# Performance work log

Measured on AMD Instinct MI355X. Metric: run time of the kernel, lower is better.

The kernel has to match this reference:

```python
import jax, jax.numpy as jnp
import numpy as np

NUM_HEADS = 8
EPS = 1e-5


def setup_inputs() -> dict:
    key = jax.random.key(0)
    ks = jax.random.split(key, 6)
    B, C, H, W = 8, 256, 32, 32
    s = 1.0 / np.sqrt(C)  # fan-in scale for 1x1 conv weights
    return {
        "x": jax.random.normal(ks[0], (B, C, H, W), jnp.float32),
        "Wq": jax.random.normal(ks[1], (C, C), jnp.float32) * s,
        "bq": jnp.zeros((C,), jnp.float32),
        "Wk": jax.random.normal(ks[2], (C, C), jnp.float32) * s,
        "bk": jnp.zeros((C,), jnp.float32),
        "Wv": jax.random.normal(ks[3], (C, C), jnp.float32) * s,
        "bv": jnp.zeros((C,), jnp.float32),
        "Wp": jax.random.normal(ks[4], (C, C), jnp.float32) * s,
        "bp": jnp.zeros((C,), jnp.float32),
        "gamma": jnp.ones((C,), jnp.float32),
        "beta": jnp.zeros((C,), jnp.float32),
    }


def _conv1x1(x, W, b):
    # 1x1 Conv2d == channel-mixing matmul: [B,C,H,W] -> [B,C,H,W]
    return jnp.einsum('oi,bihw->bohw', W, x) + b[None, :, None, None]


def reference(x, Wq, bq, Wk, bk, Wv, bv, Wp, bp, gamma, beta):
    B, C, H, W = x.shape
    nh = NUM_HEADS
    hd = C // nh
    HW = H * W

    q = _conv1x1(x, Wq, bq).reshape(B, nh, hd, HW)
    k = _conv1x1(x, Wk, bk).reshape(B, nh, hd, HW)
    v = _conv1x1(x, Wv, bv).reshape(B, nh, hd, HW)

    scores = jnp.einsum('bhdi,bhdj->bhij', q, k) / (hd ** 0.5)  # [B,nh,HW,HW]
    attn = jax.nn.softmax(scores, axis=-1)
    out = jnp.einsum('bhij,bhdj->bhdi', attn, v).reshape(B, C, H, W)

    out = _conv1x1(out, Wp, bp) + x  # residual

    # LayerNorm over channel dim (channels-last, as in original)
    o = out.transpose(0, 2, 3, 1)  # [B,H,W,C]
    mu = jnp.mean(o, axis=-1, keepdims=True)
    var = jnp.var(o, axis=-1, keepdims=True)
    o = (o - mu) * jax.lax.rsqrt(var + EPS) * gamma + beta
    return o.transpose(0, 3, 1, 2)
```

## Files before the change

kernel.cpp:

```cpp
#include <hip/hip_runtime.h>
#include <math.h>

#define NB 8
#define NC 256
#define NHW 1024
#define NHEADS 8
#define HD 32

typedef _Float16 half_t;
typedef __attribute__((ext_vector_type(8))) _Float16 half8;
typedef __attribute__((ext_vector_type(2))) _Float16 half2v;
typedef __attribute__((ext_vector_type(4))) float floatx4;

__device__ __forceinline__ half2v pk2(float a, float b) {
    union {
        __fp16 __attribute__((ext_vector_type(2))) r;
        half2v h;
    } u;
    u.r = __builtin_amdgcn_cvt_pkrtz(a, b);
    return u.h;
}
__device__ __forceinline__ void st8h(half_t* p, half2v a, half2v b) {
    union { half2v h[2]; uint2 u; } t;
    t.h[0] = a; t.h[1] = b;
    *(uint2*)p = t.u;
}

__global__ __launch_bounds__(256) void prepx(
    const float* __restrict__ Wq, const float* __restrict__ Wk,
    const float* __restrict__ Wv, const float* __restrict__ Wp,
    const float* __restrict__ x, half_t* __restrict__ Wh, half_t* __restrict__ xT)
{
    __shared__ half_t tile[64][66];
    int l = blockIdx.x;
    if (l < 256) {
        int m = l >> 6;
        const float* src = (m == 0) ? Wq : (m == 1) ? Wk : (m == 2) ? Wv : Wp;
        int off = ((l & 63) * 256 + threadIdx.x) * 4;
        float4 v = *(const float4*)&src[off];
        st8h(Wh + (size_t)m * NC * NC + off, pk2(v.x, v.y), pk2(v.z, v.w));
        return;
    }
    l -= 256;
    int t = threadIdx.x;
    int b = l >> 6;
    int i0 = ((l >> 4) & 3) * 64, s0 = (l & 15) * 64;
    const float* xb = x + ((size_t)b * NC + i0) * NHW + s0;
    int s4 = t & 15, il = t >> 4;
    #pragma unroll
    for (int r = 0; r < 4; r++) {
        int i = il + 16 * r;
        float4 v = *(const float4*)&xb[i * NHW + s4 * 4];
        *(half2v*)&tile[i][s4 * 4]     = pk2(v.x, v.y);
        *(half2v*)&tile[i][s4 * 4 + 2] = pk2(v.z, v.w);
    }
    __syncthreads();
    int iv = t & 7, sl = t >> 3;
    half_t* ob = xT + ((size_t)b * NHW + s0) * NC + i0 + iv * 8;
    #pragma unroll
    for (int r = 0; r < 2; r++) {
        int s = sl + 32 * r;
        union { half_t h[8]; int4 v4; } pkd;
        #pragma unroll
        for (int u = 0; u < 8; u++) pkd.h[u] = tile[iv * 8 + u][s];
        *(int4*)&ob[(size_t)s * NC] = pkd.v4;
    }
}

__global__ __launch_bounds__(256) void qkv_mfma(
    const half_t* __restrict__ xT, const half_t* __restrict__ Wh,
    const float* __restrict__ bq, const float* __restrict__ bk, const float* __restrict__ bv,
    half_t* __restrict__ Qt, half_t* __restrict__ Kt, half_t* __restrict__ Vv)
{
    int bz = blockIdx.z;
    int b = bz & 7, p = bz >> 3;
    const half_t* W    = Wh + (size_t)p * NC * NC;
    const float*  bias = (p == 0) ? bq : (p == 1) ? bk : bv;

    int wv = threadIdx.x >> 6, lane = threadIdx.x & 63;
    int mm = lane & 15, q = lane >> 4;
    int o0 = blockIdx.y * 64 + wv * 16;
    int s0 = blockIdx.x * 64;

    const half_t* xb = xT + (size_t)b * NHW * NC;
    floatx4 acc[4];
    #pragma unroll
    for (int nt = 0; nt < 4; nt++) acc[nt] = (floatx4){0.f, 0.f, 0.f, 0.f};

    #pragma unroll
    for (int k0 = 0; k0 < NC; k0 += 32) {
        half8 af = *(const half8*)&W[(size_t)(o0 + mm) * NC + k0 + q * 8];
        #pragma unroll
        for (int nt = 0; nt < 4; nt++) {
            half8 bf = *(const half8*)&xb[(size_t)(s0 + nt * 16 + mm) * NC + k0 + q * 8];
            acc[nt] = __builtin_amdgcn_mfma_f32_16x16x32_f16(af, bf, acc[nt], 0, 0, 0);
        }
    }

    int h  = o0 >> 5;
    int bh = b * NHEADS + h;
    int d0 = (o0 & 31) + q * 4;
    float bb[4];
    #pragma unroll
    for (int r = 0; r < 4; r++) bb[r] = bias[o0 + q * 4 + r];
    const float qs = 0.17677669529663687f;

    #pragma unroll
    for (int nt = 0; nt < 4; nt++) {
        int s = s0 + nt * 16 + mm;
        float v0 = acc[nt][0] + bb[0], v1 = acc[nt][1] + bb[1];
        float v2 = acc[nt][2] + bb[2], v3 = acc[nt][3] + bb[3];
        if (p == 0) { v0 *= qs; v1 *= qs; v2 *= qs; v3 *= qs; }
        if (p < 2) {
            half_t* out = (p == 0 ? Qt : Kt) + ((size_t)bh * NHW + s) * HD + d0;
            st8h(out, pk2(v0, v1), pk2(v2, v3));
        } else {
            Vv[((size_t)bh * HD + d0 + 0) * NHW + s] = (half_t)v0;
            Vv[((size_t)bh * HD + d0 + 1) * NHW + s] = (half_t)v1;
            Vv[((size_t)bh * HD + d0 + 2) * NHW + s] = (half_t)v2;
            Vv[((size_t)bh * HD + d0 + 3) * NHW + s] = (half_t)v3;
        }
    }
}

__global__ __launch_bounds__(256) void attn_mfma(
    const half_t* __restrict__ Qt, const half_t* __restrict__ Kt,
    const half_t* __restrict__ Vv, half_t* __restrict__ At)
{
    __shared__ half_t Pl[4][2][2][16][40];
    __shared__ float Oz[4][32][33];
    __shared__ float Dz[4][32];

    int wv = threadIdx.x >> 6, lane = threadIdx.x & 63;
    int mm = lane & 15, q = lane >> 4;
    int L = blockIdx.x;
    int bh = L & 63, iblk = L >> 6;
    int b = bh >> 3, h = bh & 7;
    int i0 = iblk * 32;

    const half_t* Qb = Qt + (size_t)bh * NHW * HD;
    const half_t* Kb = Kt + (size_t)bh * NHW * HD;
    const half_t* Vb = Vv + (size_t)bh * HD * NHW;

    half8 qf0 = *(const half8*)&Qb[(size_t)(i0 + mm) * HD + q * 8];
    half8 qf1 = *(const half8*)&Qb[(size_t)(i0 + 16 + mm) * HD + q * 8];

    const int jb = wv * 256;
    floatx4 zero = (floatx4){0.f, 0.f, 0.f, 0.f};
    floatx4 oa00 = zero, oa01 = zero, oa10 = zero, oa11 = zero;
    float d0 = 0.f, d1 = 0.f;
    const _Float16 z = (_Float16)0.f;
    half8 pf_p0 = {z, z, z, z, z, z, z, z}, pf_p1 = pf_p0;

    half8 kc0 = *(const half8*)&Kb[(size_t)(jb + mm) * HD + q * 8];
    half8 kc1 = *(const half8*)&Kb[(size_t)(jb + 16 + mm) * HD + q * 8];
    half8 kn0 = *(const half8*)&Kb[(size_t)(jb + 32 + mm) * HD + q * 8];
    half8 kn1 = *(const half8*)&Kb[(size_t)(jb + 48 + mm) * HD + q * 8];
    half8 vc0 = *(const half8*)&Vb[(size_t)mm * NHW + jb + q * 8];
    half8 vc1 = *(const half8*)&Vb[(size_t)(16 + mm) * NHW + jb + q * 8];
    half8 vp0 = vc0, vp1 = vc1;

    #pragma unroll
    for (int it = 0; it < 8; it++) {
        floatx4 s00 = __builtin_amdgcn_mfma_f32_16x16x32_f16(kc0, qf0, zero, 0, 0, 0);
        floatx4 s01 = __builtin_amdgcn_mfma_f32_16x16x32_f16(kc1, qf0, zero, 0, 0, 0);
        floatx4 s10 = __builtin_amdgcn_mfma_f32_16x16x32_f16(kc0, qf1, zero, 0, 0, 0);
        floatx4 s11 = __builtin_amdgcn_mfma_f32_16x16x32_f16(kc1, qf1, zero, 0, 0, 0);

        int jk = jb + ((it + 2) & 7) * 32;
        int jv = jb + ((it + 1) & 7) * 32;
        half8 kf0 = *(const half8*)&Kb[(size_t)(jk + mm) * HD + q * 8];
        half8 kf1 = *(const half8*)&Kb[(size_t)(jk + 16 + mm) * HD + q * 8];
        half8 vn0 = *(const half8*)&Vb[(size_t)mm * NHW + jv + q * 8];
        half8 vn1 = *(const half8*)&Vb[(size_t)(16 + mm) * NHW + jv + q * 8];

        oa00 = __builtin_amdgcn_mfma_f32_16x16x32_f16(vp0, pf_p0, oa00, 0, 0, 0);
        oa01 = __builtin_amdgcn_mfma_f32_16x16x32_f16(vp1, pf_p0, oa01, 0, 0, 0);
        oa10 = __builtin_amdgcn_mfma_f32_16x16x32_f16(vp0, pf_p1, oa10, 0, 0, 0);
        oa11 = __builtin_amdgcn_mfma_f32_16x16x32_f16(vp1, pf_p1, oa11, 0, 0, 0);

        int buf = it & 1;
        {
            float e0 = __expf(s00[0]), e1 = __expf(s00[1]);
            float e2 = __expf(s00[2]), e3 = __expf(s00[3]);
            float f0 = __expf(s01[0]), f1 = __expf(s01[1]);
            float f2 = __expf(s01[2]), f3 = __expf(s01[3]);
            d0 += ((e0 + e1) + (e2 + e3)) + ((f0 + f1) + (f2 + f3));
            half_t (*PB)[40] = Pl[wv][0][buf];
            st8h(&PB[mm][q * 4],      pk2(e0, e1), pk2(e2, e3));
            st8h(&PB[mm][16 + q * 4], pk2(f0, f1), pk2(f2, f3));
        }
        {
            float e0 = __expf(s10[0]), e1 = __expf(s10[1]);
            float e2 = __expf(s10[2]), e3 = __expf(s10[3]);
            float f0 = __expf(s11[0]), f1 = __expf(s11[1]);
            float f2 = __expf(s11[2]), f3 = __expf(s11[3]);
            d1 += ((e0 + e1) + (e2 + e3)) + ((f0 + f1) + (f2 + f3));
            half_t (*PB)[40] = Pl[wv][1][buf];
            st8h(&PB[mm][q * 4],      pk2(e0, e1), pk2(e2, e3));
            st8h(&PB[mm][16 + q * 4], pk2(f0, f1), pk2(f2, f3));
        }
        half8 pc0 = *(const half8*)&Pl[wv][0][buf][mm][q * 8];
        half8 pc1 = *(const half8*)&Pl[wv][1][buf][mm][q * 8];

        kc0 = kn0; kc1 = kn1; kn0 = kf0; kn1 = kf1;
        vp0 = vc0; vp1 = vc1; vc0 = vn0; vc1 = vn1;
        pf_p0 = pc0; pf_p1 = pc1;
    }
    oa00 = __builtin_amdgcn_mfma_f32_16x16x32_f16(vp0, pf_p0, oa00, 0, 0, 0);
    oa01 = __builtin_amdgcn_mfma_f32_16x16x32_f16(vp1, pf_p0, oa01, 0, 0, 0);
    oa10 = __builtin_amdgcn_mfma_f32_16x16x32_f16(vp0, pf_p1, oa10, 0, 0, 0);
    oa11 = __builtin_amdgcn_mfma_f32_16x16x32_f16(vp1, pf_p1, oa11, 0, 0, 0);

    d0 += __shfl_xor(d0, 16); d0 += __shfl_xor(d0, 32);
    d1 += __shfl_xor(d1, 16); d1 += __shfl_xor(d1, 32);

    #pragma unroll
    for (int r = 0; r < 4; r++) {
        Oz[wv][q * 4 + r][mm]           = oa00[r];
        Oz[wv][16 + q * 4 + r][mm]      = oa01[r];
        Oz[wv][q * 4 + r][16 + mm]      = oa10[r];
        Oz[wv][16 + q * 4 + r][16 + mm] = oa11[r];
    }
    if (q == 0) { Dz[wv][mm] = d0; Dz[wv][16 + mm] = d1; }
    __syncthreads();

    int t = threadIdx.x;
    int iloc = t >> 3, dg = t & 7;
    float den = (Dz[0][iloc] + Dz[1][iloc]) + (Dz[2][iloc] + Dz[3][iloc]);
    float rinv = 1.f / den;
    float v[4];
    #pragma unroll
    for (int r = 0; r < 4; r++) {
        int d = dg * 4 + r;
        v[r] = ((Oz[0][d][iloc] + Oz[1][d][iloc]) + (Oz[2][d][iloc] + Oz[3][d][iloc])) * rinv;
    }
    half_t* dst = At + ((size_t)b * NHW + i0 + iloc) * NC + h * HD + dg * 4;
    st8h(dst, pk2(v[0], v[1]), pk2(v[2], v[3]));
}

__global__ __launch_bounds__(512) void projln(
    const half_t* __restrict__ At, const half_t* __restrict__ Wh,
    const float* __restrict__ bp, const float* __restrict__ x,
    const float* __restrict__ gamma, const float* __restrict__ beta,
    float* __restrict__ outp)
{
    __shared__ float tile[16][273];
    __shared__ float xs[256][17];
    __shared__ float Pz[4][64][17];
    __shared__ float ps[32][16], ps2[32][16];
    __shared__ float mu_s[16], rs_s[16];

    int t = threadIdx.x, wv = t >> 6, lane = t & 63;
    int mm = lane & 15, q = lane >> 4;
    int oh = wv & 3, kh = wv >> 2;
    int o0 = oh * 64;
    int b = blockIdx.y, s0 = blockIdx.x * 16;
    const half_t* ab  = At + (size_t)b * NHW * NC;
    const half_t* Wpp = Wh + (size_t)3 * NC * NC;

    {
        int sL = t & 15, cb = t >> 4;
        #pragma unroll
        for (int pass = 0; pass < 8; pass++) {
            int c = pass * 32 + cb;
            xs[c][sL] = x[((size_t)b * NC + c) * NHW + s0 + sL];
        }
    }

    floatx4 acc[4];
    #pragma unroll
    for (int mt = 0; mt < 4; mt++) acc[mt] = (floatx4){0.f, 0.f, 0.f, 0.f};

    int kbase = kh * 128;
    #pragma unroll
    for (int kk = 0; kk < 128; kk += 32) {
        int k0 = kbase + kk;
        half8 bf = *(const half8*)&ab[(size_t)(s0 + mm) * NC + k0 + q * 8];
        #pragma unroll
        for (int mt = 0; mt < 4; mt++) {
            half8 af = *(const half8*)&Wpp[(size_t)(o0 + mt * 16 + mm) * NC + k0 + q * 8];
            acc[mt] = __builtin_amdgcn_mfma_f32_16x16x32_f16(af, bf, acc[mt], 0, 0, 0);
        }
    }

    if (kh == 1) {
        #pragma unroll
        for (int mt = 0; mt < 4; mt++)
            #pragma unroll
            for (int r = 0; r < 4; r++)
                Pz[oh][mt * 16 + q * 4 + r][mm] = acc[mt][r];
    }
    __syncthreads();
    if (kh == 0) {
        #pragma unroll
        for (int mt = 0; mt < 4; mt++) {
            #pragma unroll
            for (int r = 0; r < 4; r++) {
                int ol = mt * 16 + q * 4 + r;
                int o = o0 + ol;
                tile[mm][o] = acc[mt][r] + Pz[oh][ol][mm] + bp[o] + xs[o][mm];
            }
        }
    }
    __syncthreads();

    int sL = t & 15, part = t >> 4;
    float sum = 0.f, sq = 0.f;
    #pragma unroll
    for (int cc = 0; cc < 8; cc++) {
        float v = tile[sL][part * 8 + cc];
        sum += v; sq += v * v;
    }
    ps[part][sL] = sum; ps2[part][sL] = sq;
    __syncthreads();
    if (t < 16) {
        float S = 0.f, S2 = 0.f;
        #pragma unroll
        for (int p2 = 0; p2 < 32; p2++) { S += ps[p2][t]; S2 += ps2[p2][t]; }
        float mu  = S * (1.f / NC);
        float var = S2 * (1.f / NC) - mu * mu;
        mu_s[t] = mu;
        rs_s[t] = rsqrtf(var + 1e-5f);
    }
    __syncthreads();
    float mu = mu_s[sL], rs = rs_s[sL];
    float* ob = outp + (size_t)b * NC * NHW;
    #pragma unroll
    for (int cc = 0; cc < 8; cc++) {
        int c = part * 8 + cc;
        ob[(size_t)c * NHW + s0 + sL] = (tile[sL][c] - mu) * rs * gamma[c] + beta[c];
    }
}

extern "C" void kernel_launch(void* const* d_in, const int* in_sizes, int n_in,
                              void* d_out, int out_size, void* d_ws, size_t ws_size,
                              hipStream_t stream)
{
    const float* x     = (const float*)d_in[0];
    const float* Wq    = (const float*)d_in[1];
    const float* bq    = (const float*)d_in[2];
    const float* Wk    = (const float*)d_in[3];
    const float* bk    = (const float*)d_in[4];
    const float* Wv    = (const float*)d_in[5];
    const float* bv    = (const float*)d_in[6];
    const float* Wp    = (const float*)d_in[7];
    const float* bp    = (const float*)d_in[8];
    const float* gamma = (const float*)d_in[9];
    const float* beta  = (const float*)d_in[10];
    float* out = (float*)d_out;

    char* w = (char*)d_ws;
    half_t* xT = (half_t*)(w);
    half_t* Qt = (half_t*)(w + ((size_t)4  << 20));
    half_t* Kt = (half_t*)(w + ((size_t)8  << 20));
    half_t* Vv = (half_t*)(w + ((size_t)12 << 20));
    half_t* At = (half_t*)(w + ((size_t)16 << 20));
    half_t* Wh = (half_t*)(w + ((size_t)20 << 20));

    prepx<<<dim3(768), 256, 0, stream>>>(Wq, Wk, Wv, Wp, x, Wh, xT);
    qkv_mfma<<<dim3(16, 4, 24), 256, 0, stream>>>(xT, Wh, bq, bk, bv, Qt, Kt, Vv);
    attn_mfma<<<dim3(2048), 256, 0, stream>>>(Qt, Kt, Vv, At);
    projln<<<dim3(64, 8), 512, 0, stream>>>(At, Wh, bp, x, gamma, beta, out);
}
```

Baseline: 150.1 us.

## Merge four kernels into two persistent kernels joined by software grid barriers

Replaces the four-kernel pipeline with two persistent kernels of 768 blocks each. Inside each kernel, phases are separated by an atomic-counter grid barrier, cutting launch gaps and tail effects. The kernels change the work split: projection/LayerNorm runs unsplit per block on a subset of blocks, and attention uses a shared-memory union and a partially unrolled loop. It also folds log2(e) into the Q scale so exp2 can replace expf. The grid barrier needs all 768 blocks to be co-resident (4 per CU), or it deadlocks, and it adds a memset plus spin-wait cost.

```diff
diff --git a/kernel.cpp b/kernel.cpp
--- a/kernel.cpp
+++ b/kernel.cpp
@@ -11,6 +11,12 @@
 typedef __attribute__((ext_vector_type(8))) _Float16 half8;
 typedef __attribute__((ext_vector_type(2))) _Float16 half2v;
 typedef __attribute__((ext_vector_type(4))) float floatx4;
+
+#if __has_builtin(__builtin_amdgcn_exp2f)
+#define EXP2(x) __builtin_amdgcn_exp2f(x)
+#else
+#define EXP2(x) __expf((x) * 0.6931471805599453f)
+#endif
 
 __device__ __forceinline__ half2v pk2(float a, float b) {
     union {
@@ -26,61 +32,40 @@
     *(uint2*)p = t.u;
 }
 
-__global__ __launch_bounds__(256) void prepx(
-    const float* __restrict__ Wq, const float* __restrict__ Wk,
-    const float* __restrict__ Wv, const float* __restrict__ Wp,
-    const float* __restrict__ x, half_t* __restrict__ Wh, half_t* __restrict__ xT)
-{
-    __shared__ half_t tile[64][66];
-    int l = blockIdx.x;
-    if (l < 256) {
-        int m = l >> 6;
-        const float* src = (m == 0) ? Wq : (m == 1) ? Wk : (m == 2) ? Wv : Wp;
-        int off = ((l & 63) * 256 + threadIdx.x) * 4;
-        float4 v = *(const float4*)&src[off];
-        st8h(Wh + (size_t)m * NC * NC + off, pk2(v.x, v.y), pk2(v.z, v.w));
-        return;
-    }
-    l -= 256;
-    int t = threadIdx.x;
-    int b = l >> 6;
-    int i0 = ((l >> 4) & 3) * 64, s0 = (l & 15) * 64;
-    const float* xb = x + ((size_t)b * NC + i0) * NHW + s0;
-    int s4 = t & 15, il = t >> 4;
-    #pragma unroll
-    for (int r = 0; r < 4; r++) {
-        int i = il + 16 * r;
-        float4 v = *(const float4*)&xb[i * NHW + s4 * 4];
-        *(half2v*)&tile[i][s4 * 4]     = pk2(v.x, v.y);
-        *(half2v*)&tile[i][s4 * 4 + 2] = pk2(v.z, v.w);
-    }
-    __syncthreads();
-    int iv = t & 7, sl = t >> 3;
-    half_t* ob = xT + ((size_t)b * NHW + s0) * NC + i0 + iv * 8;
-    #pragma unroll
-    for (int r = 0; r < 2; r++) {
-        int s = sl + 32 * r;
-        union { half_t h[8]; int4 v4; } pkd;
-        #pragma unroll
-        for (int u = 0; u < 8; u++) pkd.h[u] = tile[iv * 8 + u][s];
-        *(int4*)&ob[(size_t)s * NC] = pkd.v4;
-    }
-}
-
-__global__ __launch_bounds__(256) void qkv_mfma(
+__device__ __forceinline__ void grid_barrier(unsigned* bar, unsigned nblk) {
+    __syncthreads();
+    if (threadIdx.x == 0) {
+        __threadfence();
+        __hip_atomic_fetch_add(&bar[blockIdx.x & 15], 1u,
+                               __ATOMIC_RELAXED, __HIP_MEMORY_SCOPE_AGENT);
+        for (;;) {
+            unsigned tot = 0;
+            #pragma unroll
+            for (int i = 0; i < 16; i++)
+                tot += __hip_atomic_load(&bar[i], __ATOMIC_RELAXED,
+                                         __HIP_MEMORY_SCOPE_AGENT);
+            if (tot >= nblk) break;
+            __builtin_amdgcn_s_sleep(2);
+        }
+        __threadfence();
+    }
+    __syncthreads();
+}
+
+__device__ __forceinline__ void qkv_tile(int v,
     const half_t* __restrict__ xT, const half_t* __restrict__ Wh,
     const float* __restrict__ bq, const float* __restrict__ bk, const float* __restrict__ bv,
     half_t* __restrict__ Qt, half_t* __restrict__ Kt, half_t* __restrict__ Vv)
 {
-    int bz = blockIdx.z;
-    int b = bz & 7, p = bz >> 3;
-    const half_t* W    = Wh + (size_t)p * NC * NC;
-    const float*  bias = (p == 0) ? bq : (p == 1) ? bk : bv;
+    int bx = v & 15, by = (v >> 4) & 3, bz = v >> 6;
+    int b = bz & 7, pp = bz >> 3;
+    const half_t* W    = Wh + (size_t)pp * NC * NC;
+    const float*  bias = (pp == 0) ? bq : (pp == 1) ? bk : bv;
 
     int wv = threadIdx.x >> 6, lane = threadIdx.x & 63;
     int mm = lane & 15, q = lane >> 4;
-    int o0 = blockIdx.y * 64 + wv * 16;
-    int s0 = blockIdx.x * 64;
+    int o0 = by * 64 + wv * 16;
+    int s0 = bx * 64;
 
     const half_t* xb = xT + (size_t)b * NHW * NC;
     floatx4 acc[4];
@@ -103,16 +88,16 @@
     float bb[4];
     #pragma unroll
     for (int r = 0; r < 4; r++) bb[r] = bias[o0 + q * 4 + r];
-    const float qs = 0.17677669529663687f;
+    const float qs = 0.17677669529663687f * 1.4426950408889634f;
 
     #pragma unroll
     for (int nt = 0; nt < 4; nt++) {
         int s = s0 + nt * 16 + mm;
         float v0 = acc[nt][0] + bb[0], v1 = acc[nt][1] + bb[1];
         float v2 = acc[nt][2] + bb[2], v3 = acc[nt][3] + bb[3];
-        if (p == 0) { v0 *= qs; v1 *= qs; v2 *= qs; v3 *= qs; }
-        if (p < 2) {
-            half_t* out = (p == 0 ? Qt : Kt) + ((size_t)bh * NHW + s) * HD + d0;
+        if (pp == 0) { v0 *= qs; v1 *= qs; v2 *= qs; v3 *= qs; }
+        if (pp < 2) {
+            half_t* out = (pp == 0 ? Qt : Kt) + ((size_t)bh * NHW + s) * HD + d0;
             st8h(out, pk2(v0, v1), pk2(v2, v3));
         } else {
             Vv[((size_t)bh * HD + d0 + 0) * NHW + s] = (half_t)v0;
@@ -123,18 +108,76 @@
     }
 }
 
-__global__ __launch_bounds__(256) void attn_mfma(
+__global__ __launch_bounds__(256, 4) void mega_a(
+    const float* __restrict__ Wq, const float* __restrict__ Wk,
+    const float* __restrict__ Wv, const float* __restrict__ Wp,
+    const float* __restrict__ x,
+    const float* __restrict__ bq, const float* __restrict__ bk, const float* __restrict__ bv,
+    half_t* __restrict__ Wh, half_t* __restrict__ xT,
+    half_t* __restrict__ Qt, half_t* __restrict__ Kt, half_t* __restrict__ Vv,
+    unsigned* bar)
+{
+    __shared__ half_t tile[64][66];
+    int p = blockIdx.x;
+    int t = threadIdx.x;
+
+    if (p < 512) {
+        int b = p >> 6;
+        int i0 = ((p >> 4) & 3) * 64, s0 = (p & 15) * 64;
+        const float* xb = x + ((size_t)b * NC + i0) * NHW + s0;
+        int s4 = t & 15, il = t >> 4;
+        #pragma unroll
+        for (int r = 0; r < 4; r++) {
+            int i = il + 16 * r;
+            float4 vv = *(const float4*)&xb[i * NHW + s4 * 4];
+            *(half2v*)&tile[i][s4 * 4]     = pk2(vv.x, vv.y);
+            *(half2v*)&tile[i][s4 * 4 + 2] = pk2(vv.z, vv.w);
+        }
+        __syncthreads();
+        int iv = t & 7, sl = t >> 3;
+        half_t* ob = xT + ((size_t)b * NHW + s0) * NC + i0 + iv * 8;
+        #pragma unroll
+        for (int r = 0; r < 2; r++) {
+            int s = sl + 32 * r;
+            union { half_t h[8]; int4 v4; } pkd;
+            #pragma unroll
+            for (int u = 0; u < 8; u++) pkd.h[u] = tile[iv * 8 + u][s];
+            *(int4*)&ob[(size_t)s * NC] = pkd.v4;
+        }
+    } else {
+        int l = p - 512;
+        int m = l >> 6;
+        const float* src = (m == 0) ? Wq : (m == 1) ? Wk : (m == 2) ? Wv : Wp;
+        int off = ((l & 63) * 256 + t) * 4;
+        float4 vv = *(const float4*)&src[off];
+        st8h(Wh + (size_t)m * NC * NC + off, pk2(vv.x, vv.y), pk2(vv.z, vv.w));
+    }
+
+    grid_barrier(bar, 768);
+
+    qkv_tile(p, xT, Wh, bq, bk, bv, Qt, Kt, Vv);
+    qkv_tile(p + 768, xT, Wh, bq, bk, bv, Qt, Kt, Vv);
+}
+
+struct AttnS {
+    half_t Pl[4][2][2][16][40];
+    float  Oz[4][32][33];
+    float  Dz[4][32];
+};
+struct ProjS {
+    float tile[16][273];
+    float ps[16][16], ps2[16][16];
+    float mu[16], rs[16];
+};
+union SmemB { AttnS a; ProjS pj; };
+
+__device__ __forceinline__ void attn_unit(int v, AttnS& sm,
     const half_t* __restrict__ Qt, const half_t* __restrict__ Kt,
     const half_t* __restrict__ Vv, half_t* __restrict__ At)
 {
-    __shared__ half_t Pl[4][2][2][16][40];
-    __shared__ float Oz[4][32][33];
-    __shared__ float Dz[4][32];
-
     int wv = threadIdx.x >> 6, lane = threadIdx.x & 63;
     int mm = lane & 15, q = lane >> 4;
-    int L = blockIdx.x;
-    int bh = L & 63, iblk = L >> 6;
+    int bh = v & 63, iblk = v >> 6;
     int b = bh >> 3, h = bh & 7;
     int i0 = iblk * 32;
 
@@ -160,7 +203,7 @@
     half8 vc1 = *(const half8*)&Vb[(size_t)(16 + mm) * NHW + jb + q * 8];
     half8 vp0 = vc0, vp1 = vc1;
 
-    #pragma unroll
+    #pragma unroll 2
     for (int it = 0; it < 8; it++) {
         floatx4 s00 = __builtin_amdgcn_mfma_f32_16x16x32_f16(kc0, qf0, zero, 0, 0, 0);
         floatx4 s01 = __builtin_amdgcn_mfma_f32_16x16x32_f16(kc1, qf0, zero, 0, 0, 0);
@@ -181,27 +224,27 @@
 
         int buf = it & 1;
         {
-            float e0 = __expf(s00[0]), e1 = __expf(s00[1]);
-            float e2 = __expf(s00[2]), e3 = __expf(s00[3]);
-            float f0 = __expf(s01[0]), f1 = __expf(s01[1]);
-            float f2 = __expf(s01[2]), f3 = __expf(s01[3]);
+            float e0 = EXP2(s00[0]), e1 = EXP2(s00[1]);
+            float e2 = EXP2(s00[2]), e3 = EXP2(s00[3]);
+            float f0 = EXP2(s01[0]), f1 = EXP2(s01[1]);
+            float f2 = EXP2(s01[2]), f3 = EXP2(s01[3]);
             d0 += ((e0 + e1) + (e2 + e3)) + ((f0 + f1) + (f2 + f3));
-            half_t (*PB)[40] = Pl[wv][0][buf];
+            half_t (*PB)[40] = sm.Pl[wv][0][buf];
             st8h(&PB[mm][q * 4],      pk2(e0, e1), pk2(e2, e3));
             st8h(&PB[mm][16 + q * 4], pk2(f0, f1), pk2(f2, f3));
         }
         {
-            float e0 = __expf(s10[0]), e1 = __expf(s10[1]);
-            float e2 = __expf(s10[2]), e3 = __expf(s10[3]);
-            float f0 = __expf(s11[0]), f1 = __expf(s11[1]);
-            float f2 = __expf(s11[2]), f3 = __expf(s11[3]);
+            float e0 = EXP2(s10[0]), e1 = EXP2(s10[1]);
+            float e2 = EXP2(s10[2]), e3 = EXP2(s10[3]);
+            float f0 = EXP2(s11[0]), f1 = EXP2(s11[1]);
+            float f2 = EXP2(s11[2]), f3 = EXP2(s11[3]);
             d1 += ((e0 + e1) + (e2 + e3)) + ((f0 + f1) + (f2 + f3));
-            half_t (*PB)[40] = Pl[wv][1][buf];
+            half_t (*PB)[40] = sm.Pl[wv][1][buf];
             st8h(&PB[mm][q * 4],      pk2(e0, e1), pk2(e2, e3));
             st8h(&PB[mm][16 + q * 4], pk2(f0, f1), pk2(f2, f3));
         }
-        half8 pc0 = *(const half8*)&Pl[wv][0][buf][mm][q * 8];
-        half8 pc1 = *(const half8*)&Pl[wv][1][buf][mm][q * 8];
+        half8 pc0 = *(const half8*)&sm.Pl[wv][0][buf][mm][q * 8];
+        half8 pc1 = *(const half8*)&sm.Pl[wv][1][buf][mm][q * 8];
 
         kc0 = kn0; kc1 = kn1; kn0 = kf0; kn1 = kf1;
         vp0 = vc0; vp1 = vc1; vc0 = vn0; vc1 = vn1;
@@ -217,65 +260,49 @@
 
     #pragma unroll
     for (int r = 0; r < 4; r++) {
-        Oz[wv][q * 4 + r][mm]           = oa00[r];
-        Oz[wv][16 + q * 4 + r][mm]      = oa01[r];
-        Oz[wv][q * 4 + r][16 + mm]      = oa10[r];
-        Oz[wv][16 + q * 4 + r][16 + mm] = oa11[r];
-    }
-    if (q == 0) { Dz[wv][mm] = d0; Dz[wv][16 + mm] = d1; }
+        sm.Oz[wv][q * 4 + r][mm]           = oa00[r];
+        sm.Oz[wv][16 + q * 4 + r][mm]      = oa01[r];
+        sm.Oz[wv][q * 4 + r][16 + mm]      = oa10[r];
+        sm.Oz[wv][16 + q * 4 + r][16 + mm] = oa11[r];
+    }
+    if (q == 0) { sm.Dz[wv][mm] = d0; sm.Dz[wv][16 + mm] = d1; }
     __syncthreads();
 
     int t = threadIdx.x;
     int iloc = t >> 3, dg = t & 7;
-    float den = (Dz[0][iloc] + Dz[1][iloc]) + (Dz[2][iloc] + Dz[3][iloc]);
+    float den = (sm.Dz[0][iloc] + sm.Dz[1][iloc]) + (sm.Dz[2][iloc] + sm.Dz[3][iloc]);
     float rinv = 1.f / den;
-    float v[4];
+    float vo[4];
     #pragma unroll
     for (int r = 0; r < 4; r++) {
         int d = dg * 4 + r;
-        v[r] = ((Oz[0][d][iloc] + Oz[1][d][iloc]) + (Oz[2][d][iloc] + Oz[3][d][iloc])) * rinv;
+        vo[r] = ((sm.Oz[0][d][iloc] + sm.Oz[1][d][iloc]) +
+                 (sm.Oz[2][d][iloc] + sm.Oz[3][d][iloc])) * rinv;
     }
     half_t* dst = At + ((size_t)b * NHW + i0 + iloc) * NC + h * HD + dg * 4;
-    st8h(dst, pk2(v[0], v[1]), pk2(v[2], v[3]));
-}
-
-__global__ __launch_bounds__(512) void projln(
+    st8h(dst, pk2(vo[0], vo[1]), pk2(vo[2], vo[3]));
+    __syncthreads();
+}
+
+__device__ __forceinline__ void projln_unit(int v, ProjS& sm,
     const half_t* __restrict__ At, const half_t* __restrict__ Wh,
     const float* __restrict__ bp, const float* __restrict__ x,
     const float* __restrict__ gamma, const float* __restrict__ beta,
     float* __restrict__ outp)
 {
-    __shared__ float tile[16][273];
-    __shared__ float xs[256][17];
-    __shared__ float Pz[4][64][17];
-    __shared__ float ps[32][16], ps2[32][16];
-    __shared__ float mu_s[16], rs_s[16];
-
     int t = threadIdx.x, wv = t >> 6, lane = t & 63;
     int mm = lane & 15, q = lane >> 4;
-    int oh = wv & 3, kh = wv >> 2;
-    int o0 = oh * 64;
-    int b = blockIdx.y, s0 = blockIdx.x * 16;
+    int b = v >> 6, s0 = (v & 63) * 16;
     const half_t* ab  = At + (size_t)b * NHW * NC;
     const half_t* Wpp = Wh + (size_t)3 * NC * NC;
-
-    {
-        int sL = t & 15, cb = t >> 4;
-        #pragma unroll
-        for (int pass = 0; pass < 8; pass++) {
-            int c = pass * 32 + cb;
-            xs[c][sL] = x[((size_t)b * NC + c) * NHW + s0 + sL];
-        }
-    }
+    int o0 = wv * 64;
 
     floatx4 acc[4];
     #pragma unroll
     for (int mt = 0; mt < 4; mt++) acc[mt] = (floatx4){0.f, 0.f, 0.f, 0.f};
 
-    int kbase = kh * 128;
-    #pragma unroll
-    for (int kk = 0; kk < 128; kk += 32) {
-        int k0 = kbase + kk;
+    #pragma unroll
+    for (int k0 = 0; k0 < NC; k0 += 32) {
         half8 bf = *(const half8*)&ab[(size_t)(s0 + mm) * NC + k0 + q * 8];
         #pragma unroll
         for (int mt = 0; mt < 4; mt++) {
@@ -283,24 +310,12 @@
             acc[mt] = __builtin_amdgcn_mfma_f32_16x16x32_f16(af, bf, acc[mt], 0, 0, 0);
         }
     }
-
-    if (kh == 1) {
-        #pragma unroll
-        for (int mt = 0; mt < 4; mt++)
-            #pragma unroll
-            for (int r = 0; r < 4; r++)
-                Pz[oh][mt * 16 + q * 4 + r][mm] = acc[mt][r];
-    }
-    __syncthreads();
-    if (kh == 0) {
-        #pragma unroll
-        for (int mt = 0; mt < 4; mt++) {
-            #pragma unroll
-            for (int r = 0; r < 4; r++) {
-                int ol = mt * 16 + q * 4 + r;
-                int o = o0 + ol;
-                tile[mm][o] = acc[mt][r] + Pz[oh][ol][mm] + bp[o] + xs[o][mm];
-            }
+    #pragma unroll
+    for (int mt = 0; mt < 4; mt++) {
+        #pragma unroll
+        for (int r = 0; r < 4; r++) {
+            int o = o0 + mt * 16 + q * 4 + r;
+            sm.tile[mm][o] = acc[mt][r] + bp[o] + x[((size_t)b * NC + o) * NHW + s0 + mm];
         }
     }
     __syncthreads();
@@ -308,28 +323,51 @@
     int sL = t & 15, part = t >> 4;
     float sum = 0.f, sq = 0.f;
     #pragma unroll
-    for (int cc = 0; cc < 8; cc++) {
-        float v = tile[sL][part * 8 + cc];
-        sum += v; sq += v * v;
-    }
-    ps[part][sL] = sum; ps2[part][sL] = sq;
+    for (int cc = 0; cc < 16; cc++) {
+        float vv = sm.tile[sL][part * 16 + cc];
+        sum += vv; sq += vv * vv;
+    }
+    sm.ps[part][sL] = sum; sm.ps2[part][sL] = sq;
     __syncthreads();
     if (t < 16) {
         float S = 0.f, S2 = 0.f;
         #pragma unroll
-        for (int p2 = 0; p2 < 32; p2++) { S += ps[p2][t]; S2 += ps2[p2][t]; }
-        float mu  = S * (1.f / NC);
-        float var = S2 * (1.f / NC) - mu * mu;
-        mu_s[t] = mu;
-        rs_s[t] = rsqrtf(var + 1e-5f);
-    }
-    __syncthreads();
-    float mu = mu_s[sL], rs = rs_s[sL];
+        for (int p2 = 0; p2 < 16; p2++) { S += sm.ps[p2][t]; S2 += sm.ps2[p2][t]; }
+        float muv = S * (1.f / NC);
+        float var = S2 * (1.f / NC) - muv * muv;
+        sm.mu[t] = muv;
+        sm.rs[t] = rsqrtf(var + 1e-5f);
+    }
+    __syncthreads();
+    float muv = sm.mu[sL], rsv = sm.rs[sL];
     float* ob = outp + (size_t)b * NC * NHW;
     #pragma unroll
-    for (int cc = 0; cc < 8; cc++) {
-        int c = part * 8 + cc;
-        ob[(size_t)c * NHW + s0 + sL] = (tile[sL][c] - mu) * rs * gamma[c] + beta[c];
+    for (int cc = 0; cc < 16; cc++) {
+        int c = part * 16 + cc;
+        ob[(size_t)c * NHW + s0 + sL] = (sm.tile[sL][c] - muv) * rsv * gamma[c] + beta[c];
+    }
+    __syncthreads();
+}
+
+__global__ __launch_bounds__(256, 4) void mega_b(
+    const half_t* __restrict__ Qt, const half_t* __restrict__ Kt,
+    const half_t* __restrict__ Vv, half_t* __restrict__ At,
+    const half_t* __restrict__ Wh, const float* __restrict__ bp,
+    const float* __restrict__ x, const float* __restrict__ gamma,
+    const float* __restrict__ beta, float* __restrict__ outp, unsigned* bar)
+{
+    __shared__ SmemB sm;
+    int p = blockIdx.x;
+
+    attn_unit(p, sm.a, Qt, Kt, Vv, At);
+    attn_unit(p + 768, sm.a, Qt, Kt, Vv, At);
+    if (p < 512) attn_unit(p + 1536, sm.a, Qt, Kt, Vv, At);
+
+    grid_barrier(bar, 768);
+
+    if (p >= 512) {
+        projln_unit((p - 512) * 2,     sm.pj, At, Wh, bp, x, gamma, beta, outp);
+        projln_unit((p - 512) * 2 + 1, sm.pj, At, Wh, bp, x, gamma, beta, outp);
     }
 }
 
@@ -357,9 +395,11 @@
     half_t* Vv = (half_t*)(w + ((size_t)12 << 20));
     half_t* At = (half_t*)(w + ((size_t)16 << 20));
     half_t* Wh = (half_t*)(w + ((size_t)20 << 20));
-
-    prepx<<<dim3(768), 256, 0, stream>>>(Wq, Wk, Wv, Wp, x, Wh, xT);
-    qkv_mfma<<<dim3(16, 4, 24), 256, 0, stream>>>(xT, Wh, bq, bk, bv, Qt, Kt, Vv);
-    attn_mfma<<<dim3(2048), 256, 0, stream>>>(Qt, Kt, Vv, At);
-    projln<<<dim3(64, 8), 512, 0, stream>>>(At, Wh, bp, x, gamma, beta, out);
-}
+    unsigned* bar = (unsigned*)(w + ((size_t)24 << 20));
+
+    hipMemsetAsync(bar, 0, 128, stream);
+    mega_a<<<768, 256, 0, stream>>>(Wq, Wk, Wv, Wp, x, bq, bk, bv,
+                                    Wh, xT, Qt, Kt, Vv, bar);
+    mega_b<<<768, 256, 0, stream>>>(Qt, Kt, Vv, At, Wh, bp, x, gamma, beta, out,
+                                    bar + 16);
+}
```

Result: slower. 387.9 us (+158.4%).

## Halve attention query tile to 16 rows, use exp2 with folded log2e scale

Applied to the files above, without the earlier changes.

The attention kernel now handles 16 query rows per block instead of 32 and launches twice as many blocks. Register and LDS use per block drop, and launch_bounds now asks for 6 blocks per CU to raise occupancy. The K prefetch depth is cut from two stages to one. The log2(e) factor is folded into the Q scale so the softmax can use exp2f instead of __expf. The trade-off is that each K/V tile loaded is reused across half as many queries, which doubles K/V global traffic, and half the threads sit idle in the epilogue.

```diff
diff --git a/kernel.cpp b/kernel.cpp
--- a/kernel.cpp
+++ b/kernel.cpp
@@ -11,6 +11,8 @@
 typedef __attribute__((ext_vector_type(8))) _Float16 half8;
 typedef __attribute__((ext_vector_type(2))) _Float16 half2v;
 typedef __attribute__((ext_vector_type(4))) float floatx4;
+
+#define EXP2(x) exp2f(x)
 
 __device__ __forceinline__ half2v pk2(float a, float b) {
     union {
@@ -103,7 +105,7 @@
     float bb[4];
     #pragma unroll
     for (int r = 0; r < 4; r++) bb[r] = bias[o0 + q * 4 + r];
-    const float qs = 0.17677669529663687f;
+    const float qs = 0.17677669529663687f * 1.4426950408889634f;
 
     #pragma unroll
     for (int nt = 0; nt < 4; nt++) {
@@ -123,120 +125,98 @@
     }
 }
 
-__global__ __launch_bounds__(256) void attn_mfma(
+__global__ __launch_bounds__(256, 6) void attn_mfma(
     const half_t* __restrict__ Qt, const half_t* __restrict__ Kt,
     const half_t* __restrict__ Vv, half_t* __restrict__ At)
 {
-    __shared__ half_t Pl[4][2][2][16][40];
-    __shared__ float Oz[4][32][33];
-    __shared__ float Dz[4][32];
+    __shared__ half_t Pl[4][2][16][40];
+    __shared__ float  Oz[4][32][18];
+    __shared__ float  Dz[4][16];
 
     int wv = threadIdx.x >> 6, lane = threadIdx.x & 63;
     int mm = lane & 15, q = lane >> 4;
     int L = blockIdx.x;
     int bh = L & 63, iblk = L >> 6;
     int b = bh >> 3, h = bh & 7;
-    int i0 = iblk * 32;
+    int i0 = iblk * 16;
 
     const half_t* Qb = Qt + (size_t)bh * NHW * HD;
     const half_t* Kb = Kt + (size_t)bh * NHW * HD;
     const half_t* Vb = Vv + (size_t)bh * HD * NHW;
 
-    half8 qf0 = *(const half8*)&Qb[(size_t)(i0 + mm) * HD + q * 8];
-    half8 qf1 = *(const half8*)&Qb[(size_t)(i0 + 16 + mm) * HD + q * 8];
+    half8 qf = *(const half8*)&Qb[(size_t)(i0 + mm) * HD + q * 8];
 
     const int jb = wv * 256;
     floatx4 zero = (floatx4){0.f, 0.f, 0.f, 0.f};
-    floatx4 oa00 = zero, oa01 = zero, oa10 = zero, oa11 = zero;
-    float d0 = 0.f, d1 = 0.f;
+    floatx4 oa0 = zero, oa1 = zero;
+    float dacc = 0.f;
     const _Float16 z = (_Float16)0.f;
-    half8 pf_p0 = {z, z, z, z, z, z, z, z}, pf_p1 = pf_p0;
+    half8 pf_p = {z, z, z, z, z, z, z, z};
 
     half8 kc0 = *(const half8*)&Kb[(size_t)(jb + mm) * HD + q * 8];
     half8 kc1 = *(const half8*)&Kb[(size_t)(jb + 16 + mm) * HD + q * 8];
-    half8 kn0 = *(const half8*)&Kb[(size_t)(jb + 32 + mm) * HD + q * 8];
-    half8 kn1 = *(const half8*)&Kb[(size_t)(jb + 48 + mm) * HD + q * 8];
     half8 vc0 = *(const half8*)&Vb[(size_t)mm * NHW + jb + q * 8];
     half8 vc1 = *(const half8*)&Vb[(size_t)(16 + mm) * NHW + jb + q * 8];
     half8 vp0 = vc0, vp1 = vc1;
 
     #pragma unroll
     for (int it = 0; it < 8; it++) {
-        floatx4 s00 = __builtin_amdgcn_mfma_f32_16x16x32_f16(kc0, qf0, zero, 0, 0, 0);
-        floatx4 s01 = __builtin_amdgcn_mfma_f32_16x16x32_f16(kc1, qf0, zero, 0, 0, 0);
-        floatx4 s10 = __builtin_amdgcn_mfma_f32_16x16x32_f16(kc0, qf1, zero, 0, 0, 0);
-        floatx4 s11 = __builtin_amdgcn_mfma_f32_16x16x32_f16(kc1, qf1, zero, 0, 0, 0);
-
-        int jk = jb + ((it + 2) & 7) * 32;
-        int jv = jb + ((it + 1) & 7) * 32;
-        half8 kf0 = *(const half8*)&Kb[(size_t)(jk + mm) * HD + q * 8];
-        half8 kf1 = *(const half8*)&Kb[(size_t)(jk + 16 + mm) * HD + q * 8];
-        half8 vn0 = *(const half8*)&Vb[(size_t)mm * NHW + jv + q * 8];
-        half8 vn1 = *(const half8*)&Vb[(size_t)(16 + mm) * NHW + jv + q * 8];
-
-        oa00 = __builtin_amdgcn_mfma_f32_16x16x32_f16(vp0, pf_p0, oa00, 0, 0, 0);
-        oa01 = __builtin_amdgcn_mfma_f32_16x16x32_f16(vp1, pf_p0, oa01, 0, 0, 0);
-        oa10 = __builtin_amdgcn_mfma_f32_16x16x32_f16(vp0, pf_p1, oa10, 0, 0, 0);
-        oa11 = __builtin_amdgcn_mfma_f32_16x16x32_f16(vp1, pf_p1, oa11, 0, 0, 0);
+        int jn = jb + ((it + 1) & 7) * 32;
+        half8 kf0 = *(const half8*)&Kb[(size_t)(jn + mm) * HD + q * 8];
+        half8 kf1 = *(const half8*)&Kb[(size_t)(jn + 16 + mm) * HD + q * 8];
+        half8 vn0 = *(const half8*)&Vb[(size_t)mm * NHW + jn + q * 8];
+        half8 vn1 = *(const half8*)&Vb[(size_t)(16 + mm) * NHW + jn + q * 8];
+
+        floatx4 s0 = __builtin_amdgcn_mfma_f32_16x16x32_f16(kc0, qf, zero, 0, 0, 0);
+        floatx4 s1 = __builtin_amdgcn_mfma_f32_16x16x32_f16(kc1, qf, zero, 0, 0, 0);
+
+        oa0 = __builtin_amdgcn_mfma_f32_16x16x32_f16(vp0, pf_p, oa0, 0, 0, 0);
+        oa1 = __builtin_amdgcn_mfma_f32_16x16x32_f16(vp1, pf_p, oa1, 0, 0, 0);
+
+        float e0 = EXP2(s0[0]), e1 = EXP2(s0[1]), e2 = EXP2(s0[2]), e3 = EXP2(s0[3]);
+        float f0 = EXP2(s1[0]), f1 = EXP2(s1[1]), f2 = EXP2(s1[2]), f3 = EXP2(s1[3]);
+        dacc += ((e0 + e1) + (e2 + e3)) + ((f0 + f1) + (f2 + f3));
 
         int buf = it & 1;
-        {
-            float e0 = __expf(s00[0]), e1 = __expf(s00[1]);
-            float e2 = __expf(s00[2]), e3 = __expf(s00[3]);
-            float f0 = __expf(s01[0]), f1 = __expf(s01[1]);
-            float f2 = __expf(s01[2]), f3 = __expf(s01[3]);
-            d0 += ((e0 + e1) + (e2 + e3)) + ((f0 + f1) + (f2 + f3));
-            half_t (*PB)[40] = Pl[wv][0][buf];
-            st8h(&PB[mm][q * 4],      pk2(e0, e1), pk2(e2, e3));
-            st8h(&PB[mm][16 + q * 4], pk2(f0, f1), pk2(f2, f3));
-        }
-        {
-            float e0 = __expf(s10[0]), e1 = __expf(s10[1]);
-            float e2 = __expf(s10[2]), e3 = __expf(s10[3]);
-            float f0 = __expf(s11[0]), f1 = __expf(s11[1]);
-            float f2 = __expf(s11[2]), f3 = __expf(s11[3]);
-            d1 += ((e0 + e1) + (e2 + e3)) + ((f0 + f1) + (f2 + f3));
-            half_t (*PB)[40] = Pl[wv][1][buf];
-            st8h(&PB[mm][q * 4],      pk2(e0, e1), pk2(e2, e3));
-            st8h(&PB[mm][16 + q * 4], pk2(f0, f1), pk2(f2, f3));
-        }
-        half8 pc0 = *(const half8*)&Pl[wv][0][buf][mm][q * 8];
-        half8 pc1 = *(const half8*)&Pl[wv][1][buf][mm][q * 8];
-
-        kc0 = kn0; kc1 = kn1; kn0 = kf0; kn1 = kf1;
+        half_t (*PB)[40] = Pl[wv][buf];
+        st8h(&PB[mm][q * 4],      pk2(e0, e1), pk2(e2, e3));
+        st8h(&PB[mm][16 + q * 4], pk2(f0, f1), pk2(f2, f3));
+
+        half8 pc = *(const half8*)&PB[mm][q * 8];
+
+        kc0 = kf0; kc1 = kf1;
         vp0 = vc0; vp1 = vc1; vc0 = vn0; vc1 = vn1;
-        pf_p0 = pc0; pf_p1 = pc1;
-    }
-    oa00 = __builtin_amdgcn_mfma_f32_16x16x32_f16(vp0, pf_p0, oa00, 0, 0, 0);
-    oa01 = __builtin_amdgcn_mfma_f32_16x16x32_f16(vp1, pf_p0, oa01, 0, 0, 0);
-    oa10 = __builtin_amdgcn_mfma_f32_16x16x32_f16(vp0, pf_p1, oa10, 0, 0, 0);
-    oa11 = __builtin_amdgcn_mfma_f32_16x16x32_f16(vp1, pf_p1, oa11, 0, 0, 0);
-
-    d0 += __shfl_xor(d0, 16); d0 += __shfl_xor(d0, 32);
-    d1 += __shfl_xor(d1, 16); d1 += __shfl_xor(d1, 32);
+        pf_p = pc;
+    }
+    oa0 = __builtin_amdgcn_mfma_f32_16x16x32_f16(vp0, pf_p, oa0, 0, 0, 0);
+    oa1 = __builtin_amdgcn_mfma_f32_16x16x32_f16(vp1, pf_p, oa1, 0, 0, 0);
+
+    dacc += __shfl_xor(dacc, 16);
+    dacc += __shfl_xor(dacc, 32);
 
     #pragma unroll
     for (int r = 0; r < 4; r++) {
-        Oz[wv][q * 4 + r][mm]           = oa00[r];
-        Oz[wv][16 + q * 4 + r][mm]      = oa01[r];
-        Oz[wv][q * 4 + r][16 + mm]      = oa10[r];
-        Oz[wv][16 + q * 4 + r][16 + mm] = oa11[r];
-    }
-    if (q == 0) { Dz[wv][mm] = d0; Dz[wv][16 + mm] = d1; }
+        Oz[wv][q * 4 + r][mm]      = oa0[r];
+        Oz[wv][16 + q * 4 + r][mm] = oa1[r];
+    }
+    if (q == 0) Dz[wv][mm] = dacc;
     __syncthreads();
 
     int t = threadIdx.x;
-    int iloc = t >> 3, dg = t & 7;
-    float den = (Dz[0][iloc] + Dz[1][iloc]) + (Dz[2][iloc] + Dz[3][iloc]);
-    float rinv = 1.f / den;
-    float v[4];
-    #pragma unroll
-    for (int r = 0; r < 4; r++) {
-        int d = dg * 4 + r;
-        v[r] = ((Oz[0][d][iloc] + Oz[1][d][iloc]) + (Oz[2][d][iloc] + Oz[3][d][iloc])) * rinv;
-    }
-    half_t* dst = At + ((size_t)b * NHW + i0 + iloc) * NC + h * HD + dg * 4;
-    st8h(dst, pk2(v[0], v[1]), pk2(v[2], v[3]));
+    if (t < 128) {
+        int iloc = t >> 3, dg = t & 7;
+        float den = (Dz[0][iloc] + Dz[1][iloc]) + (Dz[2][iloc] + Dz[3][iloc]);
+        float rinv = 1.f / den;
+        float vo[4];
+        #pragma unroll
+        for (int r = 0; r < 4; r++) {
+            int d = dg * 4 + r;
+            vo[r] = ((Oz[0][d][iloc] + Oz[1][d][iloc]) +
+                     (Oz[2][d][iloc] + Oz[3][d][iloc])) * rinv;
+        }
+        half_t* dst = At + ((size_t)b * NHW + i0 + iloc) * NC + h * HD + dg * 4;
+        st8h(dst, pk2(vo[0], vo[1]), pk2(vo[2], vo[3]));
+    }
 }
 
 __global__ __launch_bounds__(512) void projln(
@@ -360,6 +340,6 @@
 
     prepx<<<dim3(768), 256, 0, stream>>>(Wq, Wk, Wv, Wp, x, Wh, xT);
     qkv_mfma<<<dim3(16, 4, 24), 256, 0, stream>>>(xT, Wh, bq, bk, bv, Qt, Kt, Vv);
-    attn_mfma<<<dim3(2048), 256, 0, stream>>>(Qt, Kt, Vv, At);
+    attn_mfma<<<dim3(4096), 256, 0, stream>>>(Qt, Kt, Vv, At);
     projln<<<dim3(64, 8), 512, 0, stream>>>(At, Wh, bp, x, gamma, beta, out);
 }
```

Measured after the change: 169.9 us. 1.13x slower.

## Widen QKV register tile, fold log2e into Q scale, repad attention LDS

Applied to the files above, without the earlier changes.

The QKV projection now gives each wave a 32x64 output tile (two M-subtiles) instead of 16x64, so each loaded x fragment is reused twice and the grid halves in the y dimension. The Q scale now includes log2(e), which lets the attention kernel use exp2f in place of __expf and saves a multiply per score. The LDS padding for the P and O staging buffers is changed (40->36 halves, 33->34 floats), and P reads are split into two 8-byte loads, presumably to reduce bank conflicts. The trade-offs are higher register pressure in the QKV kernel and fewer blocks to spread across the GPU.

```diff
diff --git a/kernel.cpp b/kernel.cpp
--- a/kernel.cpp
+++ b/kernel.cpp
@@ -9,6 +9,7 @@
 
 typedef _Float16 half_t;
 typedef __attribute__((ext_vector_type(8))) _Float16 half8;
+typedef __attribute__((ext_vector_type(4))) _Float16 half4v;
 typedef __attribute__((ext_vector_type(2))) _Float16 half2v;
 typedef __attribute__((ext_vector_type(4))) float floatx4;
 
@@ -79,46 +80,57 @@
 
     int wv = threadIdx.x >> 6, lane = threadIdx.x & 63;
     int mm = lane & 15, q = lane >> 4;
-    int o0 = blockIdx.y * 64 + wv * 16;
+    int o0 = blockIdx.y * 128 + wv * 32;
     int s0 = blockIdx.x * 64;
 
     const half_t* xb = xT + (size_t)b * NHW * NC;
-    floatx4 acc[4];
-    #pragma unroll
-    for (int nt = 0; nt < 4; nt++) acc[nt] = (floatx4){0.f, 0.f, 0.f, 0.f};
+    floatx4 acc[2][4];
+    #pragma unroll
+    for (int mt = 0; mt < 2; mt++)
+        #pragma unroll
+        for (int nt = 0; nt < 4; nt++) acc[mt][nt] = (floatx4){0.f, 0.f, 0.f, 0.f};
 
     #pragma unroll
     for (int k0 = 0; k0 < NC; k0 += 32) {
-        half8 af = *(const half8*)&W[(size_t)(o0 + mm) * NC + k0 + q * 8];
+        half8 af[2], bf[4];
+        #pragma unroll
+        for (int mt = 0; mt < 2; mt++)
+            af[mt] = *(const half8*)&W[(size_t)(o0 + mt * 16 + mm) * NC + k0 + q * 8];
+        #pragma unroll
+        for (int nt = 0; nt < 4; nt++)
+            bf[nt] = *(const half8*)&xb[(size_t)(s0 + nt * 16 + mm) * NC + k0 + q * 8];
+        #pragma unroll
+        for (int mt = 0; mt < 2; mt++)
+            #pragma unroll
+            for (int nt = 0; nt < 4; nt++)
+                acc[mt][nt] = __builtin_amdgcn_mfma_f32_16x16x32_f16(af[mt], bf[nt], acc[mt][nt], 0, 0, 0);
+    }
+
+    int h  = (o0 >> 5);
+    int bh = b * NHEADS + h;
+    const float qs = 0.17677669529663687f * 1.4426950408889634f;
+
+    #pragma unroll
+    for (int mt = 0; mt < 2; mt++) {
+        int d0 = mt * 16 + q * 4;
+        float bb[4];
+        #pragma unroll
+        for (int r = 0; r < 4; r++) bb[r] = bias[o0 + mt * 16 + q * 4 + r];
         #pragma unroll
         for (int nt = 0; nt < 4; nt++) {
-            half8 bf = *(const half8*)&xb[(size_t)(s0 + nt * 16 + mm) * NC + k0 + q * 8];
-            acc[nt] = __builtin_amdgcn_mfma_f32_16x16x32_f16(af, bf, acc[nt], 0, 0, 0);
-        }
-    }
-
-    int h  = o0 >> 5;
-    int bh = b * NHEADS + h;
-    int d0 = (o0 & 31) + q * 4;
-    float bb[4];
-    #pragma unroll
-    for (int r = 0; r < 4; r++) bb[r] = bias[o0 + q * 4 + r];
-    const float qs = 0.17677669529663687f;
-
-    #pragma unroll
-    for (int nt = 0; nt < 4; nt++) {
-        int s = s0 + nt * 16 + mm;
-        float v0 = acc[nt][0] + bb[0], v1 = acc[nt][1] + bb[1];
-        float v2 = acc[nt][2] + bb[2], v3 = acc[nt][3] + bb[3];
-        if (p == 0) { v0 *= qs; v1 *= qs; v2 *= qs; v3 *= qs; }
-        if (p < 2) {
-            half_t* out = (p == 0 ? Qt : Kt) + ((size_t)bh * NHW + s) * HD + d0;
-            st8h(out, pk2(v0, v1), pk2(v2, v3));
-        } else {
-            Vv[((size_t)bh * HD + d0 + 0) * NHW + s] = (half_t)v0;
-            Vv[((size_t)bh * HD + d0 + 1) * NHW + s] = (half_t)v1;
-            Vv[((size_t)bh * HD + d0 + 2) * NHW + s] = (half_t)v2;
-            Vv[((size_t)bh * HD + d0 + 3) * NHW + s] = (half_t)v3;
+            int s = s0 + nt * 16 + mm;
+            float v0 = acc[mt][nt][0] + bb[0], v1 = acc[mt][nt][1] + bb[1];
+            float v2 = acc[mt][nt][2] + bb[2], v3 = acc[mt][nt][3] + bb[3];
+            if (p == 0) { v0 *= qs; v1 *= qs; v2 *= qs; v3 *= qs; }
+            if (p < 2) {
+                half_t* out = (p == 0 ? Qt : Kt) + ((size_t)bh * NHW + s) * HD + d0;
+                st8h(out, pk2(v0, v1), pk2(v2, v3));
+            } else {
+                Vv[((size_t)bh * HD + d0 + 0) * NHW + s] = (half_t)v0;
+                Vv[((size_t)bh * HD + d0 + 1) * NHW + s] = (half_t)v1;
+                Vv[((size_t)bh * HD + d0 + 2) * NHW + s] = (half_t)v2;
+                Vv[((size_t)bh * HD + d0 + 3) * NHW + s] = (half_t)v3;
+            }
         }
     }
 }
@@ -127,8 +139,8 @@
     const half_t* __restrict__ Qt, const half_t* __restrict__ Kt,
     const half_t* __restrict__ Vv, half_t* __restrict__ At)
 {
-    __shared__ half_t Pl[4][2][2][16][40];
-    __shared__ float Oz[4][32][33];
+    __shared__ half_t Pl[4][2][2][16][36];
+    __shared__ float Oz[4][32][34];
     __shared__ float Dz[4][32];
 
     int wv = threadIdx.x >> 6, lane = threadIdx.x & 63;
@@ -181,31 +193,34 @@
 
         int buf = it & 1;
         {
-            float e0 = __expf(s00[0]), e1 = __expf(s00[1]);
-            float e2 = __expf(s00[2]), e3 = __expf(s00[3]);
-            float f0 = __expf(s01[0]), f1 = __expf(s01[1]);
-            float f2 = __expf(s01[2]), f3 = __expf(s01[3]);
+            float e0 = exp2f(s00[0]), e1 = exp2f(s00[1]);
+            float e2 = exp2f(s00[2]), e3 = exp2f(s00[3]);
+            float f0 = exp2f(s01[0]), f1 = exp2f(s01[1]);
+            float f2 = exp2f(s01[2]), f3 = exp2f(s01[3]);
             d0 += ((e0 + e1) + (e2 + e3)) + ((f0 + f1) + (f2 + f3));
-            half_t (*PB)[40] = Pl[wv][0][buf];
+            half_t (*PB)[36] = Pl[wv][0][buf];
             st8h(&PB[mm][q * 4],      pk2(e0, e1), pk2(e2, e3));
             st8h(&PB[mm][16 + q * 4], pk2(f0, f1), pk2(f2, f3));
         }
         {
-            float e0 = __expf(s10[0]), e1 = __expf(s10[1]);
-            float e2 = __expf(s10[2]), e3 = __expf(s10[3]);
-            float f0 = __expf(s11[0]), f1 = __expf(s11[1]);
-            float f2 = __expf(s11[2]), f3 = __expf(s11[3]);
+            float e0 = exp2f(s10[0]), e1 = exp2f(s10[1]);
+            float e2 = exp2f(s10[2]), e3 = exp2f(s10[3]);
+            float f0 = exp2f(s11[0]), f1 = exp2f(s11[1]);
+            float f2 = exp2f(s11[2]), f3 = exp2f(s11[3]);
             d1 += ((e0 + e1) + (e2 + e3)) + ((f0 + f1) + (f2 + f3));
-            half_t (*PB)[40] = Pl[wv][1][buf];
+            half_t (*PB)[36] = Pl[wv][1][buf];
             st8h(&PB[mm][q * 4],      pk2(e0, e1), pk2(e2, e3));
             st8h(&PB[mm][16 + q * 4], pk2(f0, f1), pk2(f2, f3));
         }
-        half8 pc0 = *(const half8*)&Pl[wv][0][buf][mm][q * 8];
-        half8 pc1 = *(const half8*)&Pl[wv][1][buf][mm][q * 8];
+        union { half4v h4[2]; half8 h8; } u0, u1;
+        u0.h4[0] = *(half4v*)&Pl[wv][0][buf][mm][q * 8];
+        u0.h4[1] = *(half4v*)&Pl[wv][0][buf][mm][q * 8 + 4];
+        u1.h4[0] = *(half4v*)&Pl[wv][1][buf][mm][q * 8];
+        u1.h4[1] = *(half4v*)&Pl[wv][1][buf][mm][q * 8 + 4];
 
         kc0 = kn0; kc1 = kn1; kn0 = kf0; kn1 = kf1;
         vp0 = vc0; vp1 = vc1; vc0 = vn0; vc1 = vn1;
-        pf_p0 = pc0; pf_p1 = pc1;
+        pf_p0 = u0.h8; pf_p1 = u1.h8;
     }
     oa00 = __builtin_amdgcn_mfma_f32_16x16x32_f16(vp0, pf_p0, oa00, 0, 0, 0);
     oa01 = __builtin_amdgcn_mfma_f32_16x16x32_f16(vp1, pf_p0, oa01, 0, 0, 0);
@@ -359,7 +374,7 @@
     half_t* Wh = (half_t*)(w + ((size_t)20 << 20));
 
     prepx<<<dim3(768), 256, 0, stream>>>(Wq, Wk, Wv, Wp, x, Wh, xT);
-    qkv_mfma<<<dim3(16, 4, 24), 256, 0, stream>>>(xT, Wh, bq, bk, bv, Qt, Kt, Vv);
+    qkv_mfma<<<dim3(16, 2, 24), 256, 0, stream>>>(xT, Wh, bq, bk, bv, Qt, Kt, Vv);
     attn_mfma<<<dim3(2048), 256, 0, stream>>>(Qt, Kt, Vv, At);
     projln<<<dim3(64, 8), 512, 0, stream>>>(At, Wh, bp, x, gamma, beta, out);
 }
```

Measured after the change: 141.6 us. 5.7% less time.
